# Performance work log

Hardware: AMD Instinct MI355X
Metric: run time of the kernel (lower is better)

## Reference

```python
import jax, jax.numpy as jnp
import numpy as np

W_DIM = 512
IN_CH = 512
OUT_CH = 512
K = 3
PAD = K // 2
LR_MUL = 1.0
WEIGHT_GAIN = LR_MUL / np.sqrt(IN_CH * K * K)
MOD_WEIGHT_GAIN = 1.0 / np.sqrt(W_DIM)  # EqualizedLinear lr_mul=1.0
MOD_BIAS_GAIN = 1.0


def setup_inputs() -> dict:
    key = jax.random.key(0)
    k1, k2, k3, k4 = jax.random.split(key, 4)
    x = jax.random.normal(k1, (16, IN_CH, 64, 64), dtype=jnp.float32)
    w = jax.random.normal(k2, (16, W_DIM), dtype=jnp.float32)
    weight = jax.random.normal(k3, (OUT_CH, IN_CH, K, K), dtype=jnp.float32) / LR_MUL
    mod_weight = jax.random.normal(k4, (IN_CH, W_DIM), dtype=jnp.float32)
    mod_bias = jnp.ones((IN_CH,), dtype=jnp.float32)  # bias_init=1.0
    return {"x": x, "w": w, "weight": weight, "mod_weight": mod_weight, "mod_bias": mod_bias}


def _conv_one(xi, wi):
    # xi: [C_in, H, W], wi: [C_out, C_in, K, K]
    out = jax.lax.conv_general_dilated(
        xi[None], wi, window_strides=(1, 1),
        padding=[(PAD, PAD), (PAD, PAD)],
        dimension_numbers=("NCHW", "OIHW", "NCHW"))
    return out[0]


def reference(x, w, weight, mod_weight, mod_bias):
    # style = EqualizedLinear(w): [B, C_in]
    style = w @ (mod_weight * MOD_WEIGHT_GAIN).T + mod_bias * MOD_BIAS_GAIN
    # modulate weights per-sample: [B, C_out, C_in, K, K]
    wmod = (weight * WEIGHT_GAIN)[None] * style[:, None, :, None, None]
    # demodulate
    demod = jax.lax.rsqrt(jnp.sum(jnp.square(wmod), axis=(2, 3, 4), keepdims=True) + 1e-8)
    wmod = wmod * demod
    # per-sample conv (groups=batch in the original) via vmap
    out = jax.vmap(_conv_one)(x, wmod)  # [B, C_out, H, W]
    return out
```

## Files before the change

kernel.cpp:

```cpp
#include <hip/hip_runtime.h>
#include <hip/hip_bf16.h>

#define IN_CH 512
#define OUT_CH 512
#define HW 64
#define BATCH 16
#define WEIGHT_GAIN 0.014731391274719739f
#define MOD_WEIGHT_GAIN 0.04419417382415922f

#define PAD_W 66
#define XS_PIX_STRIDE 512

typedef __attribute__((ext_vector_type(8))) short frag8;
typedef __attribute__((ext_vector_type(4))) float f32x4;

__global__ void style_kernel(const float* __restrict__ w, const float* __restrict__ mw,
                             const float* __restrict__ mb, float* __restrict__ style) {
    const int gw = (blockIdx.x * 256 + threadIdx.x) >> 6;
    const int lane = threadIdx.x & 63;
    const int b = gw >> 9;
    const int i = gw & 511;
    const float4* mwp = (const float4*)(mw + (size_t)i * 512 + lane * 8);
    const float4* wp  = (const float4*)(w + (size_t)b * 512 + lane * 8);
    float4 m0 = mwp[0], m1 = mwp[1];
    float4 w0 = wp[0],  w1 = wp[1];
    float s = m0.x * w0.x + m0.y * w0.y + m0.z * w0.z + m0.w * w0.w
            + m1.x * w1.x + m1.y * w1.y + m1.z * w1.z + m1.w * w1.w;
#pragma unroll
    for (int off = 32; off > 0; off >>= 1) s += __shfl_down(s, off, 64);
    if (lane == 0) style[(size_t)b * 512 + i] = s * MOD_WEIGHT_GAIN + mb[i];
}

__global__ void wprep_kernel(const float* __restrict__ weight, float* __restrict__ wsq,
                             __hip_bfloat16* __restrict__ wbf) {
    const int idx = blockIdx.x * 256 + threadIdx.x;
    const float* wp = weight + idx * 9;
    float s = 0.f;
#pragma unroll
    for (int kk = 0; kk < 9; ++kk) {
        float v = wp[kk];
        s += v * v;
        wbf[kk * 262144 + idx] = __float2bfloat16(v);
    }
    wsq[idx] = s * (WEIGHT_GAIN * WEIGHT_GAIN);
}

__global__ void demod_kernel(const float* __restrict__ style, const float* __restrict__ wsq,
                             float* __restrict__ sc) {
    const int gw = (blockIdx.x * 256 + threadIdx.x) >> 6;
    const int lane = threadIdx.x & 63;
    const int b = gw >> 9;
    const int o = gw & 511;
    const float4* wq = (const float4*)(wsq + (size_t)o * 512 + lane * 8);
    const float4* st = (const float4*)(style + (size_t)b * 512 + lane * 8);
    float4 q0 = wq[0], q1 = wq[1];
    float4 s0 = st[0], s1 = st[1];
    float acc = q0.x * s0.x * s0.x + q0.y * s0.y * s0.y + q0.z * s0.z * s0.z + q0.w * s0.w * s0.w
              + q1.x * s1.x * s1.x + q1.y * s1.y * s1.y + q1.z * s1.z * s1.z + q1.w * s1.w * s1.w;
#pragma unroll
    for (int off = 32; off > 0; off >>= 1) acc += __shfl_down(acc, off, 64);
    if (lane == 0) sc[(size_t)b * 512 + o] = rsqrtf(acc + 1e-8f) * WEIGHT_GAIN;
}

__global__ void xs_kernel(const float* __restrict__ x, const float* __restrict__ style,
                          __hip_bfloat16* __restrict__ xsp) {
    const int y = blockIdx.x;
    const int b = blockIdx.z;
    const int t = threadIdx.x;
    const int lane = t & 63;
    const int j0 = (blockIdx.y * 4 + (t >> 6)) * 32;

    const float* xb = x + (((size_t)b * 512 + j0) * 64 + y) * 64 + lane;
    const float* stb = style + (size_t)b * 512 + j0;
    __hip_bfloat16* dst = xsp + (((size_t)b * PAD_W + (y + 1)) * PAD_W + (lane + 1)) * XS_PIX_STRIDE + j0;

    union { __hip_bfloat16 h[32]; uint4 u[4]; } pk;
#pragma unroll
    for (int k = 0; k < 32; ++k) {
        float v = xb[(size_t)k * 4096];
        pk.h[k] = __float2bfloat16(v * stb[k]);
    }
#pragma unroll
    for (int q = 0; q < 4; ++q) ((uint4*)dst)[q] = pk.u[q];
}

__global__ void border_kernel(__hip_bfloat16* __restrict__ xsp) {
    const int gw = (blockIdx.x * 256 + threadIdx.x) >> 6;
    const int lane = threadIdx.x & 63;
    const int b = gw / 260;
    const int p = gw % 260;
    int row, col;
    if (p < 66)       { row = 0;            col = p; }
    else if (p < 132) { row = 65;           col = p - 66; }
    else if (p < 196) { row = p - 132 + 1;  col = 0; }
    else              { row = p - 196 + 1;  col = 65; }
    uint4* dst = (uint4*)(xsp + (((size_t)b * PAD_W + row) * PAD_W + col) * XS_PIX_STRIDE);
    dst[lane] = uint4{0, 0, 0, 0};
}

__global__ void conv_kernel(const __hip_bfloat16* __restrict__ wbf,
                            const __hip_bfloat16* __restrict__ xsp,
                            const float* __restrict__ sc,
                            float* __restrict__ out) {
    __shared__ __hip_bfloat16 ash[128 * 64];
    __shared__ __hip_bfloat16 bsh[128 * 64];

    const int t = threadIdx.x;
    const int p0 = blockIdx.x * 128;
    const int m0 = blockIdx.y * 128;
    const int b  = blockIdx.z;
    const int y0 = p0 >> 6;

    const int r_base = t >> 3;
    const int s_slot = (t & 7) ^ (r_base & 7);
    const int aoff = (m0 + r_base) * 512 + s_slot * 8;
    int pixoff[4];
#pragma unroll
    for (int q = 0; q < 4; ++q) {
        const int rB = q * 32 + r_base;
        const int yy = y0 + (rB >> 6);
        const int xx = rB & 63;
        pixoff[q] = (((b * PAD_W) + yy) * PAD_W + xx) * XS_PIX_STRIDE + s_slot * 8;
    }

    const int wv = t >> 6;
    const int wm = (wv >> 1) * 64;
    const int wn = (wv & 1) * 64;
    const int lane = t & 63;
    const int ln15 = lane & 15;
    const int quad = lane >> 4;

    f32x4 acc[4][4] = {};

    const short* ashp = (const short*)ash;
    const short* bshp = (const short*)bsh;

    for (int kk = 0; kk < 9; ++kk) {
        const __hip_bfloat16* wsrc = wbf + kk * 262144 + aoff;
        const int shift = ((kk / 3) * PAD_W + (kk % 3)) * XS_PIX_STRIDE;
        const __hip_bfloat16* xbase = xsp + shift;

        for (int c0 = 0; c0 < 512; c0 += 64) {
#pragma unroll
            for (int q = 0; q < 4; ++q) {
                __builtin_amdgcn_global_load_lds(
                    (const __attribute__((address_space(1))) unsigned int*)(wsrc + q * 16384 + c0),
                    (__attribute__((address_space(3))) unsigned int*)((char*)ash + q * 4096 + t * 16),
                    16, 0, 0);
            }
#pragma unroll
            for (int q = 0; q < 4; ++q) {
                __builtin_amdgcn_global_load_lds(
                    (const __attribute__((address_space(1))) unsigned int*)(xbase + pixoff[q] + c0),
                    (__attribute__((address_space(3))) unsigned int*)((char*)bsh + q * 4096 + t * 16),
                    16, 0, 0);
            }
            __syncthreads();

#pragma unroll
            for (int ks = 0; ks < 2; ++ks) {
                const int gq = ks * 4 + quad;
                frag8 af[4], bfr[4];
#pragma unroll
                for (int mt = 0; mt < 4; ++mt) {
                    const int R = wm + mt * 16 + ln15;
                    af[mt] = *(const frag8*)(ashp + R * 64 + ((gq ^ (R & 7)) << 3));
                }
#pragma unroll
                for (int nt = 0; nt < 4; ++nt) {
                    const int R = wn + nt * 16 + ln15;
                    bfr[nt] = *(const frag8*)(bshp + R * 64 + ((gq ^ (R & 7)) << 3));
                }
#pragma unroll
                for (int mt = 0; mt < 4; ++mt)
#pragma unroll
                    for (int nt = 0; nt < 4; ++nt)
                        acc[mt][nt] = __builtin_amdgcn_mfma_f32_16x16x32_bf16(
                            af[mt], bfr[nt], acc[mt][nt], 0, 0, 0);
            }
            __syncthreads();
        }
    }

    const float* scb = sc + b * 512;
    float* outb = out + (size_t)b * 512 * 4096;
#pragma unroll
    for (int mt = 0; mt < 4; ++mt) {
        const int mrow = m0 + wm + mt * 16 + quad * 4;
#pragma unroll
        for (int v = 0; v < 4; ++v) {
            const float s = scb[mrow + v];
            float* orow = outb + (size_t)(mrow + v) * 4096 + p0 + wn + ln15;
#pragma unroll
            for (int nt = 0; nt < 4; ++nt)
                orow[nt * 16] = acc[mt][nt][v] * s;
        }
    }
}

extern "C" void kernel_launch(void* const* d_in, const int* in_sizes, int n_in,
                              void* d_out, int out_size, void* d_ws, size_t ws_size,
                              hipStream_t stream) {
    (void)in_sizes; (void)n_in; (void)out_size; (void)ws_size;
    const float* x      = (const float*)d_in[0];
    const float* w      = (const float*)d_in[1];
    const float* weight = (const float*)d_in[2];
    const float* mw     = (const float*)d_in[3];
    const float* mb     = (const float*)d_in[4];
    float* out = (float*)d_out;

    char* ws = (char*)d_ws;
    float* style         = (float*)(ws + 0);
    float* sc            = (float*)(ws + 32768);
    float* wsq           = (float*)(ws + 65536);
    __hip_bfloat16* wbf  = (__hip_bfloat16*)(ws + 1114112);
    __hip_bfloat16* xsp  = (__hip_bfloat16*)(ws + 5832704);

    wprep_kernel<<<dim3(1024), dim3(256), 0, stream>>>(weight, wsq, wbf);
    style_kernel<<<dim3(2048), dim3(256), 0, stream>>>(w, mw, mb, style);
    demod_kernel<<<dim3(2048), dim3(256), 0, stream>>>(style, wsq, sc);
    border_kernel<<<dim3(1040), dim3(256), 0, stream>>>(xsp);
    xs_kernel<<<dim3(64, 4, BATCH), dim3(256), 0, stream>>>(x, style, xsp);
    conv_kernel<<<dim3(32, 4, BATCH), dim3(256), 0, stream>>>(wbf, xsp, sc, out);
}
```

Before: 537.9 us.

## Triple-buffer conv GEMM with async LDS loads, larger tiles, fold border into xs

```diff
diff --git a/kernel.cpp b/kernel.cpp
--- a/kernel.cpp
+++ b/kernel.cpp
@@ -64,9 +64,24 @@
 
 __global__ void xs_kernel(const float* __restrict__ x, const float* __restrict__ style,
                           __hip_bfloat16* __restrict__ xsp) {
-    const int y = blockIdx.x;
     const int b = blockIdx.z;
     const int t = threadIdx.x;
+    if (blockIdx.x == 64) {
+        const int g = blockIdx.y;
+        const int wv = t >> 6, lane = t & 63;
+        for (int k = wv; k < 65; k += 4) {
+            const int p = g * 65 + k;
+            int row, col;
+            if (p < 66)       { row = 0;            col = p; }
+            else if (p < 132) { row = 65;           col = p - 66; }
+            else if (p < 196) { row = p - 132 + 1;  col = 0; }
+            else              { row = p - 196 + 1;  col = 65; }
+            uint4* dst = (uint4*)(xsp + (((size_t)b * PAD_W + row) * PAD_W + col) * XS_PIX_STRIDE);
+            dst[lane] = uint4{0, 0, 0, 0};
+        }
+        return;
+    }
+    const int y = blockIdx.x;
     const int lane = t & 63;
     const int j0 = (blockIdx.y * 4 + (t >> 6)) * 32;
 
@@ -84,40 +99,27 @@
     for (int q = 0; q < 4; ++q) ((uint4*)dst)[q] = pk.u[q];
 }
 
-__global__ void border_kernel(__hip_bfloat16* __restrict__ xsp) {
-    const int gw = (blockIdx.x * 256 + threadIdx.x) >> 6;
-    const int lane = threadIdx.x & 63;
-    const int b = gw / 260;
-    const int p = gw % 260;
-    int row, col;
-    if (p < 66)       { row = 0;            col = p; }
-    else if (p < 132) { row = 65;           col = p - 66; }
-    else if (p < 196) { row = p - 132 + 1;  col = 0; }
-    else              { row = p - 196 + 1;  col = 65; }
-    uint4* dst = (uint4*)(xsp + (((size_t)b * PAD_W + row) * PAD_W + col) * XS_PIX_STRIDE);
-    dst[lane] = uint4{0, 0, 0, 0};
-}
-
-__global__ void conv_kernel(const __hip_bfloat16* __restrict__ wbf,
+__global__ __launch_bounds__(512, 1) void conv_kernel(const __hip_bfloat16* __restrict__ wbf,
                             const __hip_bfloat16* __restrict__ xsp,
                             const float* __restrict__ sc,
                             float* __restrict__ out) {
-    __shared__ __hip_bfloat16 ash[128 * 64];
-    __shared__ __hip_bfloat16 bsh[128 * 64];
-
+    __shared__ char lds[147456];
+
+    const int id = blockIdx.x;
+    const int pidx = (id & 7) | (((id >> 4) & 3) << 3);
+    const int m0 = ((id >> 3) & 1) << 8;
+    const int b  = id >> 6;
+    const int p0 = pidx << 7;
+    const int y0 = p0 >> 6;
     const int t = threadIdx.x;
-    const int p0 = blockIdx.x * 128;
-    const int m0 = blockIdx.y * 128;
-    const int b  = blockIdx.z;
-    const int y0 = p0 >> 6;
 
     const int r_base = t >> 3;
     const int s_slot = (t & 7) ^ (r_base & 7);
-    const int aoff = (m0 + r_base) * 512 + s_slot * 8;
-    int pixoff[4];
-#pragma unroll
-    for (int q = 0; q < 4; ++q) {
-        const int rB = q * 32 + r_base;
+    const size_t abase = (size_t)(m0 + r_base) * 512 + s_slot * 8;
+    int pixoff[2];
+#pragma unroll
+    for (int q = 0; q < 2; ++q) {
+        const int rB = q * 64 + r_base;
         const int yy = y0 + (rB >> 6);
         const int xx = rB & 63;
         pixoff[q] = (((b * PAD_W) + yy) * PAD_W + xx) * XS_PIX_STRIDE + s_slot * 8;
@@ -132,55 +134,78 @@
 
     f32x4 acc[4][4] = {};
 
-    const short* ashp = (const short*)ash;
-    const short* bshp = (const short*)bsh;
-
-    for (int kk = 0; kk < 9; ++kk) {
-        const __hip_bfloat16* wsrc = wbf + kk * 262144 + aoff;
-        const int shift = ((kk / 3) * PAD_W + (kk % 3)) * XS_PIX_STRIDE;
-        const __hip_bfloat16* xbase = xsp + shift;
-
-        for (int c0 = 0; c0 < 512; c0 += 64) {
-#pragma unroll
-            for (int q = 0; q < 4; ++q) {
-                __builtin_amdgcn_global_load_lds(
-                    (const __attribute__((address_space(1))) unsigned int*)(wsrc + q * 16384 + c0),
-                    (__attribute__((address_space(3))) unsigned int*)((char*)ash + q * 4096 + t * 16),
-                    16, 0, 0);
-            }
-#pragma unroll
-            for (int q = 0; q < 4; ++q) {
-                __builtin_amdgcn_global_load_lds(
-                    (const __attribute__((address_space(1))) unsigned int*)(xbase + pixoff[q] + c0),
-                    (__attribute__((address_space(3))) unsigned int*)((char*)bsh + q * 4096 + t * 16),
-                    16, 0, 0);
-            }
-            __syncthreads();
-
-#pragma unroll
-            for (int ks = 0; ks < 2; ++ks) {
-                const int gq = ks * 4 + quad;
-                frag8 af[4], bfr[4];
-#pragma unroll
-                for (int mt = 0; mt < 4; ++mt) {
-                    const int R = wm + mt * 16 + ln15;
-                    af[mt] = *(const frag8*)(ashp + R * 64 + ((gq ^ (R & 7)) << 3));
-                }
-#pragma unroll
-                for (int nt = 0; nt < 4; ++nt) {
-                    const int R = wn + nt * 16 + ln15;
-                    bfr[nt] = *(const frag8*)(bshp + R * 64 + ((gq ^ (R & 7)) << 3));
-                }
-#pragma unroll
-                for (int mt = 0; mt < 4; ++mt)
-#pragma unroll
-                    for (int nt = 0; nt < 4; ++nt)
-                        acc[mt][nt] = __builtin_amdgcn_mfma_f32_16x16x32_bf16(
-                            af[mt], bfr[nt], acc[mt][nt], 0, 0, 0);
-            }
-            __syncthreads();
-        }
-    }
+#define STAGE(S, R) do {                                                              \
+    const int kk_ = (S) >> 3;                                                         \
+    const int c0_ = ((S) & 7) << 6;                                                   \
+    const __hip_bfloat16* wsrc_ = wbf + kk_ * 262144 + abase + c0_;                   \
+    char* Ab_ = lds + (R) * 49152;                                                    \
+    _Pragma("unroll")                                                                 \
+    for (int q = 0; q < 4; ++q)                                                       \
+        __builtin_amdgcn_global_load_lds(                                             \
+            (const __attribute__((address_space(1))) unsigned int*)(wsrc_ + q * 32768),\
+            (__attribute__((address_space(3))) unsigned int*)(Ab_ + q * 8192 + t * 16),\
+            16, 0, 0);                                                                \
+    const int shift_ = ((kk_ / 3) * PAD_W + (kk_ % 3)) * XS_PIX_STRIDE;               \
+    const __hip_bfloat16* xb_ = xsp + shift_ + c0_;                                   \
+    char* Bb_ = lds + (R) * 49152 + 32768;                                            \
+    _Pragma("unroll")                                                                 \
+    for (int q = 0; q < 2; ++q)                                                       \
+        __builtin_amdgcn_global_load_lds(                                             \
+            (const __attribute__((address_space(1))) unsigned int*)(xb_ + pixoff[q]), \
+            (__attribute__((address_space(3))) unsigned int*)(Bb_ + q * 8192 + t * 16),\
+            16, 0, 0);                                                                \
+} while (0)
+
+#define COMPUTE(R) do {                                                               \
+    const short* Ap_ = (const short*)(lds + (R) * 49152);                             \
+    const short* Bp_ = (const short*)(lds + (R) * 49152 + 32768);                     \
+    _Pragma("unroll")                                                                 \
+    for (int ks = 0; ks < 2; ++ks) {                                                  \
+        const int gq = ks * 4 + quad;                                                 \
+        frag8 af[4], bfr[4];                                                          \
+        _Pragma("unroll")                                                             \
+        for (int mt = 0; mt < 4; ++mt) {                                              \
+            const int R_ = wm + mt * 16 + ln15;                                       \
+            af[mt] = *(const frag8*)(Ap_ + R_ * 64 + ((gq ^ (R_ & 7)) << 3));         \
+        }                                                                             \
+        _Pragma("unroll")                                                             \
+        for (int nt = 0; nt < 4; ++nt) {                                              \
+            const int R_ = wn + nt * 16 + ln15;                                       \
+            bfr[nt] = *(const frag8*)(Bp_ + R_ * 64 + ((gq ^ (R_ & 7)) << 3));        \
+        }                                                                             \
+        __builtin_amdgcn_s_setprio(1);                                                \
+        _Pragma("unroll")                                                             \
+        for (int mt = 0; mt < 4; ++mt)                                                \
+            _Pragma("unroll")                                                         \
+            for (int nt = 0; nt < 4; ++nt)                                            \
+                acc[mt][nt] = __builtin_amdgcn_mfma_f32_16x16x32_bf16(                \
+                    af[mt], bfr[nt], acc[mt][nt], 0, 0, 0);                           \
+        __builtin_amdgcn_s_setprio(0);                                                \
+    }                                                                                 \
+} while (0)
+
+#define WAIT6 asm volatile("s_waitcnt vmcnt(6)" ::: "memory")
+#define BAR   asm volatile("s_barrier" ::: "memory")
+
+#define ITER_S(RC, RS) do { WAIT6; BAR; STAGE(s + 2, RS); COMPUTE(RC); BAR; ++s; } while (0)
+#define ITER_N(RC)     do { WAIT6; BAR;                   COMPUTE(RC); BAR; ++s; } while (0)
+
+    STAGE(0, 0);
+    STAGE(1, 1);
+    int s = 0;
+    while (s < 69) { ITER_S(0, 2); ITER_S(1, 0); ITER_S(2, 1); }
+    ITER_S(0, 2);
+    ITER_N(1);
+    asm volatile("s_waitcnt vmcnt(0)" ::: "memory");
+    BAR;
+    COMPUTE(2);
+
+#undef ITER_S
+#undef ITER_N
+#undef WAIT6
+#undef BAR
+#undef STAGE
+#undef COMPUTE
 
     const float* scb = sc + b * 512;
     float* outb = out + (size_t)b * 512 * 4096;
@@ -189,11 +214,11 @@
         const int mrow = m0 + wm + mt * 16 + quad * 4;
 #pragma unroll
         for (int v = 0; v < 4; ++v) {
-            const float s = scb[mrow + v];
+            const float sv = scb[mrow + v];
             float* orow = outb + (size_t)(mrow + v) * 4096 + p0 + wn + ln15;
 #pragma unroll
             for (int nt = 0; nt < 4; ++nt)
-                orow[nt * 16] = acc[mt][nt][v] * s;
+                orow[nt * 16] = acc[mt][nt][v] * sv;
         }
     }
 }
@@ -219,7 +244,6 @@
     wprep_kernel<<<dim3(1024), dim3(256), 0, stream>>>(weight, wsq, wbf);
     style_kernel<<<dim3(2048), dim3(256), 0, stream>>>(w, mw, mb, style);
     demod_kernel<<<dim3(2048), dim3(256), 0, stream>>>(style, wsq, sc);
-    border_kernel<<<dim3(1040), dim3(256), 0, stream>>>(xsp);
-    xs_kernel<<<dim3(64, 4, BATCH), dim3(256), 0, stream>>>(x, style, xsp);
-    conv_kernel<<<dim3(32, 4, BATCH), dim3(256), 0, stream>>>(wbf, xsp, sc, out);
-}
+    xs_kernel<<<dim3(65, 4, BATCH), dim3(256), 0, stream>>>(x, style, xsp);
+    conv_kernel<<<dim3(1024), dim3(512), 0, stream>>>(wbf, xsp, sc, out);
+}
```

Measured after the change: 536.1 us. No clear change (-0.3%).
